# Performance work log

Hardware: AMD Instinct MI355X
Metric: run time of the kernel (lower is better)

The kernel has to match this reference:

```python
import jax, jax.numpy as jnp
import numpy as np

B, D, N, C = 8192, 128, 64, 256

def setup_inputs() -> dict:
    key = jax.random.key(0)
    ks = jax.random.split(key, 7)
    s1 = 1.0 / np.sqrt(D)
    s2 = 1.0 / np.sqrt(C)
    return {
        "X": jax.random.normal(ks[0], (B, D, N), dtype=jnp.float32),
        "W1": jax.random.normal(ks[1], (D, C), dtype=jnp.float32) * s1,
        "b1": jax.random.normal(ks[2], (C,), dtype=jnp.float32) * s1,
        "W2": jax.random.normal(ks[3], (C, C), dtype=jnp.float32) * s2,
        "b2": jax.random.normal(ks[4], (C,), dtype=jnp.float32) * s2,
        "W3": jax.random.normal(ks[5], (C, 1), dtype=jnp.float32) * s2,
        "b3": jax.random.normal(ks[6], (1,), dtype=jnp.float32) * s2,
    }

def reference(X, W1, b1, W2, b2, W3, b3):
    # X: (B, D, N); each per-node slice X[:, :, i] goes through the shared MLP.
    # Batched over nodes: one GEMM instead of N tiny launches.
    h = jax.nn.relu(jnp.einsum('bdn,dc->bnc', X, W1) + b1)   # (B, N, C)
    h = jax.nn.relu(jnp.einsum('bnc,ce->bne', h, W2) + b2)   # (B, N, C)
    logits = jnp.einsum('bnc,co->bno', h, W3) + b3           # (B, N, 1)
    logits = logits[..., 0]                                   # (B, N)
    zeros = jnp.zeros((X.shape[0], 1), dtype=logits.dtype)    # add_zero=True
    return jnp.concatenate([zeros, logits], axis=1)           # (B, N+1)
```

## Files before the change

### kernel.cpp

```cpp
#include <hip/hip_runtime.h>
#include <hip/hip_bf16.h>

typedef unsigned short u16;
typedef unsigned int   u32;
typedef __attribute__((ext_vector_type(8))) short bf16x8;
typedef __attribute__((ext_vector_type(4))) float f32x4;

#define NB 8192

__device__ __forceinline__ u32 pack2bf(float a, float b) {
    __hip_bfloat162 h = __float22bfloat162_rn(make_float2(a, b));
    return *reinterpret_cast<u32*>(&h);
}

__device__ __forceinline__ u16 f2bf(float x) {
    u32 u = __float_as_uint(x);
    u32 r = u + 0x7FFFu + ((u >> 16) & 1u);
    return (u16)(r >> 16);
}

__global__ __launch_bounds__(256) void prep_weights(
    const float* __restrict__ W1, const float* __restrict__ W2,
    u16* __restrict__ w1fr, u16* __restrict__ w2fr)
{
    int tid = blockIdx.x * 256 + threadIdx.x;
    if (tid < 32768) {
        const int f = tid >> 9, r = tid & 511, l = r >> 3, j = r & 7;
        const int wv = f >> 4, mt = (f >> 2) & 3, ks = f & 3;
        const int c = 64 * wv + 16 * mt + (l & 15);
        const int d = 32 * ks + 8 * (l >> 4) + j;
        w1fr[tid] = f2bf(W1[d * 256 + c]);
    } else {
        const int t2 = tid - 32768;
        if (t2 < 65536) {
            const int f = t2 >> 9, r = t2 & 511, l = r >> 3, j = r & 7;
            const int wv = f >> 5, et = (f >> 3) & 3, ks = f & 7;
            const int e = 64 * wv + 16 * et + (l & 15);
            const int c = 32 * ks + 8 * (l >> 4) + j;
            w2fr[t2] = f2bf(W2[c * 256 + e]);
        }
    }
}

__global__ __launch_bounds__(256, 4) void fused_mlp(
    const float* __restrict__ X,
    const float* __restrict__ b1, const float* __restrict__ b2,
    const float* __restrict__ W3, const float* __restrict__ b3,
    const u16* __restrict__ w1fr, const u16* __restrict__ w2fr,
    float* __restrict__ out)
{
    __shared__ u16 smem[64 * 256];
    u16* xt   = smem;
    u16* h1s  = smem;
    float* partl = (float*)smem;

    const int tid = threadIdx.x;
    const int w   = tid >> 6;
    const int l   = tid & 63;
    const int lc  = l & 15;
    const int lk  = l >> 4;
    const int b   = blockIdx.x;
    const float* Xb = X + (size_t)b * 8192;

    const u16* w1b = w1fr + w * 8192  + l * 8;
    const u16* w2b = w2fr + w * 16384 + l * 8;

    #pragma unroll
    for (int it = 0; it < 4; ++it) {
        const int dc = w + 4 * it, d0 = dc << 3;
        float v[8];
        #pragma unroll
        for (int j = 0; j < 8; ++j) v[j] = Xb[(d0 + j) * 64 + l];
        u32 pk[4];
        #pragma unroll
        for (int j = 0; j < 4; ++j) pk[j] = pack2bf(v[2 * j], v[2 * j + 1]);
        *(uint4*)(xt + l * 128 + ((dc ^ lc) << 3)) = make_uint4(pk[0], pk[1], pk[2], pk[3]);
    }

    bf16x8 afrN[4];
    #pragma unroll
    for (int mt = 0; mt < 4; ++mt)
        afrN[mt] = *(const bf16x8*)(w1b + mt * 2048);
    __syncthreads();

    f32x4 acc[4][4];
    #pragma unroll
    for (int mt = 0; mt < 4; ++mt)
        #pragma unroll
        for (int nt = 0; nt < 4; ++nt) acc[mt][nt] = (f32x4){0.f, 0.f, 0.f, 0.f};

    #pragma unroll
    for (int ks = 0; ks < 4; ++ks) {
        bf16x8 afr[4], bfr[4];
        #pragma unroll
        for (int mt = 0; mt < 4; ++mt) afr[mt] = afrN[mt];
        if (ks < 3) {
            #pragma unroll
            for (int mt = 0; mt < 4; ++mt)
                afrN[mt] = *(const bf16x8*)(w1b + (mt * 4 + ks + 1) * 512);
        }
        #pragma unroll
        for (int nt = 0; nt < 4; ++nt)
            bfr[nt] = *(const bf16x8*)(xt + (16 * nt + lc) * 128 + (((4 * ks + lk) ^ lc) << 3));
        #pragma unroll
        for (int mt = 0; mt < 4; ++mt)
            #pragma unroll
            for (int nt = 0; nt < 4; ++nt)
                acc[mt][nt] = __builtin_amdgcn_mfma_f32_16x16x32_bf16(afr[mt], bfr[nt], acc[mt][nt], 0, 0, 0);
    }
    __syncthreads();

    #pragma unroll
    for (int mt = 0; mt < 4; ++mt) {
        const int c0 = 64 * w + 16 * mt + 4 * lk;
        const float4 bv = *(const float4*)(b1 + c0);
        #pragma unroll
        for (int nt = 0; nt < 4; ++nt) {
            const int n = 16 * nt + lc;
            float x0 = fmaxf(acc[mt][nt][0] + bv.x, 0.f);
            float x1 = fmaxf(acc[mt][nt][1] + bv.y, 0.f);
            float x2 = fmaxf(acc[mt][nt][2] + bv.z, 0.f);
            float x3 = fmaxf(acc[mt][nt][3] + bv.w, 0.f);
            const int chunk = (c0 >> 3) ^ lc;
            *(uint2*)(h1s + n * 256 + (chunk << 3) + (c0 & 7)) =
                make_uint2(pack2bf(x0, x1), pack2bf(x2, x3));
        }
    }

    bf16x8 bfrN[4];
    #pragma unroll
    for (int nt = 0; nt < 4; ++nt)
        bfrN[nt] = *(const bf16x8*)(w2b + nt * 4096);
    __syncthreads();

    f32x4 acc2[4][4];
    #pragma unroll
    for (int mt = 0; mt < 4; ++mt)
        #pragma unroll
        for (int nt = 0; nt < 4; ++nt) acc2[mt][nt] = (f32x4){0.f, 0.f, 0.f, 0.f};

    #pragma unroll
    for (int ks = 0; ks < 8; ++ks) {
        bf16x8 afr[4], bfr[4];
        #pragma unroll
        for (int nt = 0; nt < 4; ++nt) bfr[nt] = bfrN[nt];
        if (ks < 7) {
            #pragma unroll
            for (int nt = 0; nt < 4; ++nt)
                bfrN[nt] = *(const bf16x8*)(w2b + (nt * 8 + ks + 1) * 512);
        }
        #pragma unroll
        for (int mt = 0; mt < 4; ++mt)
            afr[mt] = *(const bf16x8*)(h1s + (16 * mt + lc) * 256 + (((4 * ks + lk) ^ lc) << 3));
        #pragma unroll
        for (int mt = 0; mt < 4; ++mt)
            #pragma unroll
            for (int nt = 0; nt < 4; ++nt)
                acc2[mt][nt] = __builtin_amdgcn_mfma_f32_16x16x32_bf16(afr[mt], bfr[nt], acc2[mt][nt], 0, 0, 0);
    }
    __syncthreads();

    float b2v[4], w3v[4];
    #pragma unroll
    for (int nt = 0; nt < 4; ++nt) {
        const int e = 64 * w + 16 * nt + lc;
        b2v[nt] = b2[e];
        w3v[nt] = W3[e];
    }
    #pragma unroll
    for (int mt = 0; mt < 4; ++mt) {
        #pragma unroll
        for (int j = 0; j < 4; ++j) {
            float s = 0.f;
            #pragma unroll
            for (int nt = 0; nt < 4; ++nt)
                s += fmaxf(acc2[mt][nt][j] + b2v[nt], 0.f) * w3v[nt];
            s += __shfl_xor(s, 1);
            s += __shfl_xor(s, 2);
            s += __shfl_xor(s, 4);
            s += __shfl_xor(s, 8);
            if (lc == 0) partl[w * 64 + 16 * mt + 4 * lk + j] = s;
        }
    }
    __syncthreads();

    if (tid < 64) {
        float s = partl[0 * 64 + tid] + partl[1 * 64 + tid] + partl[2 * 64 + tid] + partl[3 * 64 + tid] + b3[0];
        out[(size_t)b * 65 + 1 + tid] = s;
    } else if (tid == 64) {
        out[(size_t)b * 65] = 0.f;
    }
}

extern "C" void kernel_launch(void* const* d_in, const int* in_sizes, int n_in,
                              void* d_out, int out_size, void* d_ws, size_t ws_size,
                              hipStream_t stream) {
    const float* X  = (const float*)d_in[0];
    const float* W1 = (const float*)d_in[1];
    const float* b1 = (const float*)d_in[2];
    const float* W2 = (const float*)d_in[3];
    const float* b2 = (const float*)d_in[4];
    const float* W3 = (const float*)d_in[5];
    const float* b3 = (const float*)d_in[6];
    float* out = (float*)d_out;

    u16* w1fr = (u16*)d_ws;
    u16* w2fr = w1fr + 32768;

    prep_weights<<<384, 256, 0, stream>>>(W1, W2, w1fr, w2fr);
    fused_mlp<<<NB, 256, 0, stream>>>(X, b1, b2, W3, b3, w1fr, w2fr, out);
}
```

Before: 122.2 us.

## Make fused MLP persistent with async global-to-LDS prefetch of next batch

Turns the one-block-per-batch kernel into a persistent kernel with 512 blocks, each looping over 16 batch elements. The next X tile is prefetched straight into LDS with global_load_lds while layer 2 runs, and the bf16 conversion moves into the layer-1 fragment reads. Biases are folded into the accumulator initial values, and MFMA sections get raised wave priority. The aim is to hide X load latency and per-block startup cost, in exchange for more LDS use (fp32 X tile plus a separate h1 buffer), occupancy lowered to 2 blocks, and more LDS reads with conversion inside the GEMM loop.

```diff
diff --git a/kernel.cpp b/kernel.cpp
--- a/kernel.cpp
+++ b/kernel.cpp
@@ -6,7 +6,9 @@
 typedef __attribute__((ext_vector_type(8))) short bf16x8;
 typedef __attribute__((ext_vector_type(4))) float f32x4;
 
-#define NB 8192
+#define NB     8192
+#define GRID_P 512
+#define ITERS  (NB / GRID_P)
 
 __device__ __forceinline__ u32 pack2bf(float a, float b) {
     __hip_bfloat162 h = __float22bfloat162_rn(make_float2(a, b));
@@ -42,124 +44,33 @@
     }
 }
 
-__global__ __launch_bounds__(256, 4) void fused_mlp(
+__global__ __launch_bounds__(256, 2) void fused_mlp(
     const float* __restrict__ X,
     const float* __restrict__ b1, const float* __restrict__ b2,
     const float* __restrict__ W3, const float* __restrict__ b3,
     const u16* __restrict__ w1fr, const u16* __restrict__ w2fr,
     float* __restrict__ out)
 {
-    __shared__ u16 smem[64 * 256];
-    u16* xt   = smem;
-    u16* h1s  = smem;
-    float* partl = (float*)smem;
+    __shared__ __align__(16) float xs[64 * 128];
+    __shared__ __align__(16) u16   h1s[64 * 256];
+    __shared__ float partl[4][64];
 
     const int tid = threadIdx.x;
     const int w   = tid >> 6;
     const int l   = tid & 63;
     const int lc  = l & 15;
     const int lk  = l >> 4;
-    const int b   = blockIdx.x;
-    const float* Xb = X + (size_t)b * 8192;
 
     const u16* w1b = w1fr + w * 8192  + l * 8;
     const u16* w2b = w2fr + w * 16384 + l * 8;
 
-    #pragma unroll
-    for (int it = 0; it < 4; ++it) {
-        const int dc = w + 4 * it, d0 = dc << 3;
-        float v[8];
-        #pragma unroll
-        for (int j = 0; j < 8; ++j) v[j] = Xb[(d0 + j) * 64 + l];
-        u32 pk[4];
-        #pragma unroll
-        for (int j = 0; j < 4; ++j) pk[j] = pack2bf(v[2 * j], v[2 * j + 1]);
-        *(uint4*)(xt + l * 128 + ((dc ^ lc) << 3)) = make_uint4(pk[0], pk[1], pk[2], pk[3]);
-    }
-
-    bf16x8 afrN[4];
+    const int dl = w * 4 + (l >> 4);
+    const int m0 = (l & 15) * 4;
+
+    float4 b1q[4];
     #pragma unroll
     for (int mt = 0; mt < 4; ++mt)
-        afrN[mt] = *(const bf16x8*)(w1b + mt * 2048);
-    __syncthreads();
-
-    f32x4 acc[4][4];
-    #pragma unroll
-    for (int mt = 0; mt < 4; ++mt)
-        #pragma unroll
-        for (int nt = 0; nt < 4; ++nt) acc[mt][nt] = (f32x4){0.f, 0.f, 0.f, 0.f};
-
-    #pragma unroll
-    for (int ks = 0; ks < 4; ++ks) {
-        bf16x8 afr[4], bfr[4];
-        #pragma unroll
-        for (int mt = 0; mt < 4; ++mt) afr[mt] = afrN[mt];
-        if (ks < 3) {
-            #pragma unroll
-            for (int mt = 0; mt < 4; ++mt)
-                afrN[mt] = *(const bf16x8*)(w1b + (mt * 4 + ks + 1) * 512);
-        }
-        #pragma unroll
-        for (int nt = 0; nt < 4; ++nt)
-            bfr[nt] = *(const bf16x8*)(xt + (16 * nt + lc) * 128 + (((4 * ks + lk) ^ lc) << 3));
-        #pragma unroll
-        for (int mt = 0; mt < 4; ++mt)
-            #pragma unroll
-            for (int nt = 0; nt < 4; ++nt)
-                acc[mt][nt] = __builtin_amdgcn_mfma_f32_16x16x32_bf16(afr[mt], bfr[nt], acc[mt][nt], 0, 0, 0);
-    }
-    __syncthreads();
-
-    #pragma unroll
-    for (int mt = 0; mt < 4; ++mt) {
-        const int c0 = 64 * w + 16 * mt + 4 * lk;
-        const float4 bv = *(const float4*)(b1 + c0);
-        #pragma unroll
-        for (int nt = 0; nt < 4; ++nt) {
-            const int n = 16 * nt + lc;
-            float x0 = fmaxf(acc[mt][nt][0] + bv.x, 0.f);
-            float x1 = fmaxf(acc[mt][nt][1] + bv.y, 0.f);
-            float x2 = fmaxf(acc[mt][nt][2] + bv.z, 0.f);
-            float x3 = fmaxf(acc[mt][nt][3] + bv.w, 0.f);
-            const int chunk = (c0 >> 3) ^ lc;
-            *(uint2*)(h1s + n * 256 + (chunk << 3) + (c0 & 7)) =
-                make_uint2(pack2bf(x0, x1), pack2bf(x2, x3));
-        }
-    }
-
-    bf16x8 bfrN[4];
-    #pragma unroll
-    for (int nt = 0; nt < 4; ++nt)
-        bfrN[nt] = *(const bf16x8*)(w2b + nt * 4096);
-    __syncthreads();
-
-    f32x4 acc2[4][4];
-    #pragma unroll
-    for (int mt = 0; mt < 4; ++mt)
-        #pragma unroll
-        for (int nt = 0; nt < 4; ++nt) acc2[mt][nt] = (f32x4){0.f, 0.f, 0.f, 0.f};
-
-    #pragma unroll
-    for (int ks = 0; ks < 8; ++ks) {
-        bf16x8 afr[4], bfr[4];
-        #pragma unroll
-        for (int nt = 0; nt < 4; ++nt) bfr[nt] = bfrN[nt];
-        if (ks < 7) {
-            #pragma unroll
-            for (int nt = 0; nt < 4; ++nt)
-                bfrN[nt] = *(const bf16x8*)(w2b + (nt * 8 + ks + 1) * 512);
-        }
-        #pragma unroll
-        for (int mt = 0; mt < 4; ++mt)
-            afr[mt] = *(const bf16x8*)(h1s + (16 * mt + lc) * 256 + (((4 * ks + lk) ^ lc) << 3));
-        #pragma unroll
-        for (int mt = 0; mt < 4; ++mt)
-            #pragma unroll
-            for (int nt = 0; nt < 4; ++nt)
-                acc2[mt][nt] = __builtin_amdgcn_mfma_f32_16x16x32_bf16(afr[mt], bfr[nt], acc2[mt][nt], 0, 0, 0);
-    }
-    __syncthreads();
-
+        b1q[mt] = *(const float4*)(b1 + 64 * w + 16 * mt + 4 * lk);
     float b2v[4], w3v[4];
     #pragma unroll
     for (int nt = 0; nt < 4; ++nt) {
@@ -167,28 +78,166 @@
         b2v[nt] = b2[e];
         w3v[nt] = W3[e];
     }
-    #pragma unroll
-    for (int mt = 0; mt < 4; ++mt) {
-        #pragma unroll
-        for (int j = 0; j < 4; ++j) {
-            float s = 0.f;
+    const float b3v = b3[0];
+
+    int b = blockIdx.x;
+    {
+        const float* Xb = X + (size_t)b * 8192;
+        #pragma unroll
+        for (int i = 0; i < 8; ++i) {
+            const int d = i * 16 + dl;
+            const float* src = Xb + d * 64 + (m0 ^ (((d >> 3) & 1) << 4));
+            __builtin_amdgcn_global_load_lds(
+                (const __attribute__((address_space(1))) void*)src,
+                (__attribute__((address_space(3))) void*)(xs + i * 1024 + w * 256 + (l & 63) * 4),
+                16, 0, 0);
+        }
+    }
+    __syncthreads();
+
+    #pragma unroll 1
+    for (int it = 0; it < ITERS; ++it, b += GRID_P) {
+        f32x4 acc[4][4];
+        #pragma unroll
+        for (int mt = 0; mt < 4; ++mt)
             #pragma unroll
             for (int nt = 0; nt < 4; ++nt)
-                s += fmaxf(acc2[mt][nt][j] + b2v[nt], 0.f) * w3v[nt];
-            s += __shfl_xor(s, 1);
-            s += __shfl_xor(s, 2);
-            s += __shfl_xor(s, 4);
-            s += __shfl_xor(s, 8);
-            if (lc == 0) partl[w * 64 + 16 * mt + 4 * lk + j] = s;
-        }
-    }
-    __syncthreads();
-
-    if (tid < 64) {
-        float s = partl[0 * 64 + tid] + partl[1 * 64 + tid] + partl[2 * 64 + tid] + partl[3 * 64 + tid] + b3[0];
-        out[(size_t)b * 65 + 1 + tid] = s;
-    } else if (tid == 64) {
-        out[(size_t)b * 65] = 0.f;
+                acc[mt][nt] = (f32x4){b1q[mt].x, b1q[mt].y, b1q[mt].z, b1q[mt].w};
+
+        bf16x8 afrN[4];
+        #pragma unroll
+        for (int mt = 0; mt < 4; ++mt)
+            afrN[mt] = *(const bf16x8*)(w1b + mt * 2048);
+
+        const int px = (lk & 1) << 4;
+        #pragma unroll
+        for (int ks = 0; ks < 4; ++ks) {
+            bf16x8 afr[4], bfr[4];
+            #pragma unroll
+            for (int mt = 0; mt < 4; ++mt) afr[mt] = afrN[mt];
+            if (ks < 3) {
+                #pragma unroll
+                for (int mt = 0; mt < 4; ++mt)
+                    afrN[mt] = *(const bf16x8*)(w1b + (mt * 4 + ks + 1) * 512);
+            }
+            #pragma unroll
+            for (int nt = 0; nt < 4; ++nt) {
+                const int col = (16 * nt + lc) ^ px;
+                const int rb  = (32 * ks + 8 * lk) * 64 + col;
+                float xv[8];
+                #pragma unroll
+                for (int j = 0; j < 8; ++j) xv[j] = xs[rb + j * 64];
+                union { bf16x8 v; u32 d[4]; } fr;
+                #pragma unroll
+                for (int j = 0; j < 4; ++j) fr.d[j] = pack2bf(xv[2 * j], xv[2 * j + 1]);
+                bfr[nt] = fr.v;
+            }
+            __builtin_amdgcn_s_setprio(1);
+            #pragma unroll
+            for (int mt = 0; mt < 4; ++mt)
+                #pragma unroll
+                for (int nt = 0; nt < 4; ++nt)
+                    acc[mt][nt] = __builtin_amdgcn_mfma_f32_16x16x32_bf16(afr[mt], bfr[nt], acc[mt][nt], 0, 0, 0);
+            __builtin_amdgcn_s_setprio(0);
+        }
+        __syncthreads();
+
+        const int bn = b + GRID_P;
+        if (bn < NB) {
+            const float* Xb = X + (size_t)bn * 8192;
+            #pragma unroll
+            for (int i = 0; i < 8; ++i) {
+                const int d = i * 16 + dl;
+                const float* src = Xb + d * 64 + (m0 ^ (((d >> 3) & 1) << 4));
+                __builtin_amdgcn_global_load_lds(
+                    (const __attribute__((address_space(1))) void*)src,
+                    (__attribute__((address_space(3))) void*)(xs + i * 1024 + w * 256 + (l & 63) * 4),
+                    16, 0, 0);
+            }
+        }
+
+        #pragma unroll
+        for (int mt = 0; mt < 4; ++mt) {
+            const int c0 = 64 * w + 16 * mt + 4 * lk;
+            #pragma unroll
+            for (int nt = 0; nt < 4; ++nt) {
+                const int n = 16 * nt + lc;
+                float x0 = fmaxf(acc[mt][nt][0], 0.f);
+                float x1 = fmaxf(acc[mt][nt][1], 0.f);
+                float x2 = fmaxf(acc[mt][nt][2], 0.f);
+                float x3 = fmaxf(acc[mt][nt][3], 0.f);
+                const int chunk = (c0 >> 3) ^ lc;
+                *(uint2*)(h1s + n * 256 + (chunk << 3) + (c0 & 7)) =
+                    make_uint2(pack2bf(x0, x1), pack2bf(x2, x3));
+            }
+        }
+
+        asm volatile("s_waitcnt lgkmcnt(0)" ::: "memory");
+        __builtin_amdgcn_s_barrier();
+        asm volatile("" ::: "memory");
+
+        f32x4 acc2[4][4];
+        #pragma unroll
+        for (int mt = 0; mt < 4; ++mt)
+            #pragma unroll
+            for (int nt = 0; nt < 4; ++nt)
+                acc2[mt][nt] = (f32x4){b2v[nt], b2v[nt], b2v[nt], b2v[nt]};
+
+        bf16x8 bfrN[4];
+        #pragma unroll
+        for (int nt = 0; nt < 4; ++nt)
+            bfrN[nt] = *(const bf16x8*)(w2b + nt * 4096);
+
+        #pragma unroll
+        for (int ks = 0; ks < 8; ++ks) {
+            bf16x8 afr[4], bfr[4];
+            #pragma unroll
+            for (int nt = 0; nt < 4; ++nt) bfr[nt] = bfrN[nt];
+            if (ks < 7) {
+                #pragma unroll
+                for (int nt = 0; nt < 4; ++nt)
+                    bfrN[nt] = *(const bf16x8*)(w2b + (nt * 8 + ks + 1) * 512);
+            }
+            #pragma unroll
+            for (int mt = 0; mt < 4; ++mt)
+                afr[mt] = *(const bf16x8*)(h1s + (16 * mt + lc) * 256 + (((4 * ks + lk) ^ lc) << 3));
+            __builtin_amdgcn_s_setprio(1);
+            #pragma unroll
+            for (int mt = 0; mt < 4; ++mt)
+                #pragma unroll
+                for (int nt = 0; nt < 4; ++nt)
+                    acc2[mt][nt] = __builtin_amdgcn_mfma_f32_16x16x32_bf16(afr[mt], bfr[nt], acc2[mt][nt], 0, 0, 0);
+            __builtin_amdgcn_s_setprio(0);
+        }
+
+        #pragma unroll
+        for (int mt = 0; mt < 4; ++mt) {
+            #pragma unroll
+            for (int j = 0; j < 4; ++j) {
+                float s = 0.f;
+                #pragma unroll
+                for (int nt = 0; nt < 4; ++nt)
+                    s += fmaxf(acc2[mt][nt][j], 0.f) * w3v[nt];
+                s += __shfl_xor(s, 1);
+                s += __shfl_xor(s, 2);
+                s += __shfl_xor(s, 4);
+                s += __shfl_xor(s, 8);
+                if (lc == 0) partl[w][16 * mt + 4 * lk + j] = s;
+            }
+        }
+
+        asm volatile("s_waitcnt lgkmcnt(0)" ::: "memory");
+        __builtin_amdgcn_s_barrier();
+        asm volatile("" ::: "memory");
+
+        if (tid < 64) {
+            float s = partl[0][tid] + partl[1][tid] + partl[2][tid] + partl[3][tid] + b3v;
+            out[(size_t)b * 65 + 1 + tid] = s;
+        } else if (tid == 64) {
+            out[(size_t)b * 65] = 0.f;
+        }
+
+        __syncthreads();
     }
 }
 
@@ -208,5 +257,5 @@
     u16* w2fr = w1fr + 32768;
 
     prep_weights<<<384, 256, 0, stream>>>(W1, W2, w1fr, w2fr);
-    fused_mlp<<<NB, 256, 0, stream>>>(X, b1, b2, W3, b3, w1fr, w2fr, out);
-}
+    fused_mlp<<<GRID_P, 256, 0, stream>>>(X, b1, b2, W3, b3, w1fr, w2fr, out);
+}
```

Result: slower. 302.5 us (+147.6%).

## Convert fused MLP into persistent producer/consumer warp-specialized pipeline

Applied to the files above, without the earlier changes.

Replaces the one-block-per-batch kernel with 256 persistent 1024-thread blocks that loop over batches. Even waves compute layer 1 and prefetch the next X tile into a double-buffered LDS slot. Odd waves compute layer 2 plus the W3 reduction on the previous h1 buffer, and one wave writes the output two steps behind. Biases are folded into the accumulator initialisation and MFMA sections are marked with setprio. The aim is to overlap X loading with matrix math, but it uses 100KB of LDS per block, only 256 blocks on the device, and a block-wide barrier every step.

```diff
diff --git a/kernel.cpp b/kernel.cpp
--- a/kernel.cpp
+++ b/kernel.cpp
@@ -6,7 +6,9 @@
 typedef __attribute__((ext_vector_type(8))) short bf16x8;
 typedef __attribute__((ext_vector_type(4))) float f32x4;
 
-#define NB 8192
+#define NB    8192
+#define NBLK  256
+#define STEPS (NB / NBLK)
 
 __device__ __forceinline__ u32 pack2bf(float a, float b) {
     __hip_bfloat162 h = __float22bfloat162_rn(make_float2(a, b));
@@ -26,169 +28,213 @@
     int tid = blockIdx.x * 256 + threadIdx.x;
     if (tid < 32768) {
         const int f = tid >> 9, r = tid & 511, l = r >> 3, j = r & 7;
-        const int wv = f >> 4, mt = (f >> 2) & 3, ks = f & 3;
-        const int c = 64 * wv + 16 * mt + (l & 15);
+        const int p = f >> 3, mt = (f >> 2) & 1, ks = f & 3;
+        const int c = 32 * p + 16 * mt + (l & 15);
         const int d = 32 * ks + 8 * (l >> 4) + j;
         w1fr[tid] = f2bf(W1[d * 256 + c]);
     } else {
         const int t2 = tid - 32768;
         if (t2 < 65536) {
             const int f = t2 >> 9, r = t2 & 511, l = r >> 3, j = r & 7;
-            const int wv = f >> 5, et = (f >> 3) & 3, ks = f & 7;
-            const int e = 64 * wv + 16 * et + (l & 15);
-            const int c = 32 * ks + 8 * (l >> 4) + j;
-            w2fr[t2] = f2bf(W2[c * 256 + e]);
-        }
-    }
-}
-
-__global__ __launch_bounds__(256, 4) void fused_mlp(
+            const int q = f >> 4, et = (f >> 3) & 1, ks = f & 7;
+            const int e = 32 * q + 16 * et + (l & 15);
+            const int cc = 32 * ks + 8 * (l >> 4) + j;
+            w2fr[t2] = f2bf(W2[cc * 256 + e]);
+        }
+    }
+}
+
+__global__ __launch_bounds__(1024, 4) void pc_mlp(
     const float* __restrict__ X,
     const float* __restrict__ b1, const float* __restrict__ b2,
     const float* __restrict__ W3, const float* __restrict__ b3,
     const u16* __restrict__ w1fr, const u16* __restrict__ w2fr,
     float* __restrict__ out)
 {
-    __shared__ u16 smem[64 * 256];
-    u16* xt   = smem;
-    u16* h1s  = smem;
-    float* partl = (float*)smem;
+    extern __shared__ __align__(16) u16 smem[];
+    u16*   const xt0   = smem;
+    u16*   const h10   = smem + 16384;
+    float* const partl = (float*)(smem + 49152);
 
     const int tid = threadIdx.x;
-    const int w   = tid >> 6;
+    const int wv  = tid >> 6;
     const int l   = tid & 63;
     const int lc  = l & 15;
     const int lk  = l >> 4;
-    const int b   = blockIdx.x;
-    const float* Xb = X + (size_t)b * 8192;
-
-    const u16* w1b = w1fr + w * 8192  + l * 8;
-    const u16* w2b = w2fr + w * 16384 + l * 8;
-
-    #pragma unroll
-    for (int it = 0; it < 4; ++it) {
-        const int dc = w + 4 * it, d0 = dc << 3;
-        float v[8];
+    const bool isProd = (wv & 1) == 0;
+    const int rid = wv >> 1;
+    const int bk  = blockIdx.x;
+
+    float4 b1q[2];
+    const u16* w1b = w1fr + rid * 4096 + l * 8;
+    float b2v[2], w3v[2];
+    const u16* w2b = w2fr + rid * 8192 + l * 8;
+    float b3v = 0.f;
+    if (isProd) {
         #pragma unroll
-        for (int j = 0; j < 8; ++j) v[j] = Xb[(d0 + j) * 64 + l];
-        u32 pk[4];
+        for (int mt = 0; mt < 2; ++mt)
+            b1q[mt] = *(const float4*)(b1 + 32 * rid + 16 * mt + 4 * lk);
+    } else {
         #pragma unroll
-        for (int j = 0; j < 4; ++j) pk[j] = pack2bf(v[2 * j], v[2 * j + 1]);
-        *(uint4*)(xt + l * 128 + ((dc ^ lc) << 3)) = make_uint4(pk[0], pk[1], pk[2], pk[3]);
-    }
-
-    bf16x8 afrN[4];
-    #pragma unroll
-    for (int mt = 0; mt < 4; ++mt)
-        afrN[mt] = *(const bf16x8*)(w1b + mt * 2048);
+        for (int et = 0; et < 2; ++et) {
+            const int e = 32 * rid + 16 * et + lc;
+            b2v[et] = b2[e];
+            w3v[et] = W3[e];
+        }
+        b3v = b3[0];
+    }
+
+    if (isProd) {
+        const float* Xb = X + (size_t)bk * 8192;
+        #pragma unroll
+        for (int c2 = 0; c2 < 2; ++c2) {
+            const int dc = rid + 8 * c2, d0 = dc << 3;
+            float v[8];
+            #pragma unroll
+            for (int j = 0; j < 8; ++j) v[j] = Xb[(d0 + j) * 64 + l];
+            u32 pk[4];
+            #pragma unroll
+            for (int j = 0; j < 4; ++j) pk[j] = pack2bf(v[2 * j], v[2 * j + 1]);
+            *(uint4*)(xt0 + l * 128 + ((dc ^ lc) << 3)) = make_uint4(pk[0], pk[1], pk[2], pk[3]);
+        }
+    }
     __syncthreads();
 
-    f32x4 acc[4][4];
-    #pragma unroll
-    for (int mt = 0; mt < 4; ++mt)
-        #pragma unroll
-        for (int nt = 0; nt < 4; ++nt) acc[mt][nt] = (f32x4){0.f, 0.f, 0.f, 0.f};
-
-    #pragma unroll
-    for (int ks = 0; ks < 4; ++ks) {
-        bf16x8 afr[4], bfr[4];
-        #pragma unroll
-        for (int mt = 0; mt < 4; ++mt) afr[mt] = afrN[mt];
-        if (ks < 3) {
-            #pragma unroll
-            for (int mt = 0; mt < 4; ++mt)
-                afrN[mt] = *(const bf16x8*)(w1b + (mt * 4 + ks + 1) * 512);
-        }
-        #pragma unroll
-        for (int nt = 0; nt < 4; ++nt)
-            bfr[nt] = *(const bf16x8*)(xt + (16 * nt + lc) * 128 + (((4 * ks + lk) ^ lc) << 3));
-        #pragma unroll
-        for (int mt = 0; mt < 4; ++mt)
-            #pragma unroll
-            for (int nt = 0; nt < 4; ++nt)
-                acc[mt][nt] = __builtin_amdgcn_mfma_f32_16x16x32_bf16(afr[mt], bfr[nt], acc[mt][nt], 0, 0, 0);
-    }
-    __syncthreads();
-
-    #pragma unroll
-    for (int mt = 0; mt < 4; ++mt) {
-        const int c0 = 64 * w + 16 * mt + 4 * lk;
-        const float4 bv = *(const float4*)(b1 + c0);
-        #pragma unroll
-        for (int nt = 0; nt < 4; ++nt) {
-            const int n = 16 * nt + lc;
-            float x0 = fmaxf(acc[mt][nt][0] + bv.x, 0.f);
-            float x1 = fmaxf(acc[mt][nt][1] + bv.y, 0.f);
-            float x2 = fmaxf(acc[mt][nt][2] + bv.z, 0.f);
-            float x3 = fmaxf(acc[mt][nt][3] + bv.w, 0.f);
-            const int chunk = (c0 >> 3) ^ lc;
-            *(uint2*)(h1s + n * 256 + (chunk << 3) + (c0 & 7)) =
-                make_uint2(pack2bf(x0, x1), pack2bf(x2, x3));
-        }
-    }
-
-    bf16x8 bfrN[4];
-    #pragma unroll
-    for (int nt = 0; nt < 4; ++nt)
-        bfrN[nt] = *(const bf16x8*)(w2b + nt * 4096);
-    __syncthreads();
-
-    f32x4 acc2[4][4];
-    #pragma unroll
-    for (int mt = 0; mt < 4; ++mt)
-        #pragma unroll
-        for (int nt = 0; nt < 4; ++nt) acc2[mt][nt] = (f32x4){0.f, 0.f, 0.f, 0.f};
-
-    #pragma unroll
-    for (int ks = 0; ks < 8; ++ks) {
-        bf16x8 afr[4], bfr[4];
-        #pragma unroll
-        for (int nt = 0; nt < 4; ++nt) bfr[nt] = bfrN[nt];
-        if (ks < 7) {
-            #pragma unroll
-            for (int nt = 0; nt < 4; ++nt)
-                bfrN[nt] = *(const bf16x8*)(w2b + (nt * 8 + ks + 1) * 512);
-        }
-        #pragma unroll
-        for (int mt = 0; mt < 4; ++mt)
-            afr[mt] = *(const bf16x8*)(h1s + (16 * mt + lc) * 256 + (((4 * ks + lk) ^ lc) << 3));
-        #pragma unroll
-        for (int mt = 0; mt < 4; ++mt)
-            #pragma unroll
-            for (int nt = 0; nt < 4; ++nt)
-                acc2[mt][nt] = __builtin_amdgcn_mfma_f32_16x16x32_bf16(afr[mt], bfr[nt], acc2[mt][nt], 0, 0, 0);
-    }
-    __syncthreads();
-
-    float b2v[4], w3v[4];
-    #pragma unroll
-    for (int nt = 0; nt < 4; ++nt) {
-        const int e = 64 * w + 16 * nt + lc;
-        b2v[nt] = b2[e];
-        w3v[nt] = W3[e];
-    }
-    #pragma unroll
-    for (int mt = 0; mt < 4; ++mt) {
-        #pragma unroll
-        for (int j = 0; j < 4; ++j) {
-            float s = 0.f;
-            #pragma unroll
-            for (int nt = 0; nt < 4; ++nt)
-                s += fmaxf(acc2[mt][nt][j] + b2v[nt], 0.f) * w3v[nt];
-            s += __shfl_xor(s, 1);
-            s += __shfl_xor(s, 2);
-            s += __shfl_xor(s, 4);
-            s += __shfl_xor(s, 8);
-            if (lc == 0) partl[w * 64 + 16 * mt + 4 * lk + j] = s;
-        }
-    }
-    __syncthreads();
-
-    if (tid < 64) {
-        float s = partl[0 * 64 + tid] + partl[1 * 64 + tid] + partl[2 * 64 + tid] + partl[3 * 64 + tid] + b3[0];
-        out[(size_t)b * 65 + 1 + tid] = s;
-    } else if (tid == 64) {
-        out[(size_t)b * 65] = 0.f;
+    #pragma unroll 1
+    for (int it = 0; it < STEPS + 2; ++it) {
+        if (isProd) {
+            if (it < STEPS) {
+                const int b = bk + it * NBLK;
+                float v[2][8];
+                if (it < STEPS - 1) {
+                    const float* Xn = X + (size_t)(b + NBLK) * 8192;
+                    #pragma unroll
+                    for (int c2 = 0; c2 < 2; ++c2) {
+                        const int d0 = (rid + 8 * c2) << 3;
+                        #pragma unroll
+                        for (int j = 0; j < 8; ++j) v[c2][j] = Xn[(d0 + j) * 64 + l];
+                    }
+                }
+                const u16* xb = xt0 + (it & 1) * 8192;
+                f32x4 acc[2][4];
+                #pragma unroll
+                for (int mt = 0; mt < 2; ++mt)
+                    #pragma unroll
+                    for (int nt = 0; nt < 4; ++nt)
+                        acc[mt][nt] = (f32x4){b1q[mt].x, b1q[mt].y, b1q[mt].z, b1q[mt].w};
+                bf16x8 afrN[2];
+                #pragma unroll
+                for (int mt = 0; mt < 2; ++mt)
+                    afrN[mt] = *(const bf16x8*)(w1b + mt * 2048);
+                #pragma unroll
+                for (int ks = 0; ks < 4; ++ks) {
+                    bf16x8 afr[2], bfr[4];
+                    #pragma unroll
+                    for (int mt = 0; mt < 2; ++mt) afr[mt] = afrN[mt];
+                    if (ks < 3) {
+                        #pragma unroll
+                        for (int mt = 0; mt < 2; ++mt)
+                            afrN[mt] = *(const bf16x8*)(w1b + (mt * 4 + ks + 1) * 512);
+                    }
+                    #pragma unroll
+                    for (int nt = 0; nt < 4; ++nt)
+                        bfr[nt] = *(const bf16x8*)(xb + (16 * nt + lc) * 128 + (((4 * ks + lk) ^ lc) << 3));
+                    __builtin_amdgcn_s_setprio(1);
+                    #pragma unroll
+                    for (int mt = 0; mt < 2; ++mt)
+                        #pragma unroll
+                        for (int nt = 0; nt < 4; ++nt)
+                            acc[mt][nt] = __builtin_amdgcn_mfma_f32_16x16x32_bf16(afr[mt], bfr[nt], acc[mt][nt], 0, 0, 0);
+                    __builtin_amdgcn_s_setprio(0);
+                }
+                u16* hw = h10 + (it & 1) * 16384;
+                #pragma unroll
+                for (int mt = 0; mt < 2; ++mt) {
+                    const int c0 = 32 * rid + 16 * mt + 4 * lk;
+                    #pragma unroll
+                    for (int nt = 0; nt < 4; ++nt) {
+                        const int n = 16 * nt + lc;
+                        float x0 = fmaxf(acc[mt][nt][0], 0.f);
+                        float x1 = fmaxf(acc[mt][nt][1], 0.f);
+                        float x2 = fmaxf(acc[mt][nt][2], 0.f);
+                        float x3 = fmaxf(acc[mt][nt][3], 0.f);
+                        const int chunk = (c0 >> 3) ^ lc;
+                        *(uint2*)(hw + n * 256 + (chunk << 3) + (c0 & 7)) =
+                            make_uint2(pack2bf(x0, x1), pack2bf(x2, x3));
+                    }
+                }
+                if (it < STEPS - 1) {
+                    u16* xn = xt0 + ((it + 1) & 1) * 8192;
+                    #pragma unroll
+                    for (int c2 = 0; c2 < 2; ++c2) {
+                        const int dc = rid + 8 * c2;
+                        u32 pk[4];
+                        #pragma unroll
+                        for (int j = 0; j < 4; ++j) pk[j] = pack2bf(v[c2][2 * j], v[c2][2 * j + 1]);
+                        *(uint4*)(xn + l * 128 + ((dc ^ lc) << 3)) = make_uint4(pk[0], pk[1], pk[2], pk[3]);
+                    }
+                }
+            }
+        } else {
+            if (it >= 2 && it <= STEPS + 1 && wv == 1) {
+                const int bo = bk + (it - 2) * NBLK;
+                const float* pr = partl + ((it - 1) & 1) * 512;
+                float s = b3v;
+                #pragma unroll
+                for (int k = 0; k < 8; ++k) s += pr[k * 64 + l];
+                out[(size_t)bo * 65 + 1 + l] = s;
+                if (l == 0) out[(size_t)bo * 65] = 0.f;
+            }
+            if (it >= 1 && it <= STEPS) {
+                const u16* hb = h10 + ((it - 1) & 1) * 16384;
+                f32x4 acc2[4][2];
+                #pragma unroll
+                for (int mt = 0; mt < 4; ++mt)
+                    #pragma unroll
+                    for (int et = 0; et < 2; ++et)
+                        acc2[mt][et] = (f32x4){b2v[et], b2v[et], b2v[et], b2v[et]};
+                bf16x8 bfrN[2];
+                #pragma unroll
+                for (int et = 0; et < 2; ++et)
+                    bfrN[et] = *(const bf16x8*)(w2b + et * 4096);
+                #pragma unroll
+                for (int ks = 0; ks < 8; ++ks) {
+                    bf16x8 afr[4], bfr[2];
+                    #pragma unroll
+                    for (int et = 0; et < 2; ++et) bfr[et] = bfrN[et];
+                    if (ks < 7) {
+                        #pragma unroll
+                        for (int et = 0; et < 2; ++et)
+                            bfrN[et] = *(const bf16x8*)(w2b + (et * 8 + ks + 1) * 512);
+                    }
+                    #pragma unroll
+                    for (int mt = 0; mt < 4; ++mt)
+                        afr[mt] = *(const bf16x8*)(hb + (16 * mt + lc) * 256 + (((4 * ks + lk) ^ lc) << 3));
+                    __builtin_amdgcn_s_setprio(1);
+                    #pragma unroll
+                    for (int mt = 0; mt < 4; ++mt)
+                        #pragma unroll
+                        for (int et = 0; et < 2; ++et)
+                            acc2[mt][et] = __builtin_amdgcn_mfma_f32_16x16x32_bf16(afr[mt], bfr[et], acc2[mt][et], 0, 0, 0);
+                    __builtin_amdgcn_s_setprio(0);
+                }
+                float* pw = partl + (it & 1) * 512 + rid * 64;
+                #pragma unroll
+                for (int mt = 0; mt < 4; ++mt) {
+                    #pragma unroll
+                    for (int j = 0; j < 4; ++j) {
+                        float s = fmaxf(acc2[mt][0][j], 0.f) * w3v[0]
+                                + fmaxf(acc2[mt][1][j], 0.f) * w3v[1];
+                        s += __shfl_xor(s, 1);
+                        s += __shfl_xor(s, 2);
+                        s += __shfl_xor(s, 4);
+                        s += __shfl_xor(s, 8);
+                        if (lc == 0) pw[16 * mt + 4 * lk + j] = s;
+                    }
+                }
+            }
+        }
+        __syncthreads();
     }
 }
 
@@ -208,5 +254,5 @@
     u16* w2fr = w1fr + 32768;
 
     prep_weights<<<384, 256, 0, stream>>>(W1, W2, w1fr, w2fr);
-    fused_mlp<<<NB, 256, 0, stream>>>(X, b1, b2, W3, b3, w1fr, w2fr, out);
-}
+    pc_mlp<<<NBLK, 1024, 102400, stream>>>(X, b1, b2, W3, b3, w1fr, w2fr, out);
+}
```

Result: slower. 447.8 us (+266.6%).

## Load X fragments directly into registers, skipping LDS staging; fold biases into accumulators

Applied to the files above, without the earlier changes.

The first GEMM now builds its X operand fragments straight from global memory in registers. Each 32-d slice is converted to bf16 and fed to MFMA as it arrives, so the LDS transpose buffer and two barriers are gone. Biases b1 and b2 are preloaded into the accumulators instead of being added in the epilogue, and partl gets its own shared array. In exchange, every wave re-reads the whole X tile from global/L2, four times the global traffic per block, with strided 4-byte loads. The grid size is also derived from the input size.

```diff
diff --git a/kernel.cpp b/kernel.cpp
--- a/kernel.cpp
+++ b/kernel.cpp
@@ -49,10 +49,8 @@
     const u16* __restrict__ w1fr, const u16* __restrict__ w2fr,
     float* __restrict__ out)
 {
-    __shared__ u16 smem[64 * 256];
-    u16* xt   = smem;
-    u16* h1s  = smem;
-    float* partl = (float*)smem;
+    __shared__ __align__(16) u16 h1s[64 * 256];
+    __shared__ float partl[4][64];
 
     const int tid = threadIdx.x;
     const int w   = tid >> 6;
@@ -65,79 +63,82 @@
     const u16* w1b = w1fr + w * 8192  + l * 8;
     const u16* w2b = w2fr + w * 16384 + l * 8;
 
-    #pragma unroll
-    for (int it = 0; it < 4; ++it) {
-        const int dc = w + 4 * it, d0 = dc << 3;
-        float v[8];
-        #pragma unroll
-        for (int j = 0; j < 8; ++j) v[j] = Xb[(d0 + j) * 64 + l];
-        u32 pk[4];
-        #pragma unroll
-        for (int j = 0; j < 4; ++j) pk[j] = pack2bf(v[2 * j], v[2 * j + 1]);
-        *(uint4*)(xt + l * 128 + ((dc ^ lc) << 3)) = make_uint4(pk[0], pk[1], pk[2], pk[3]);
-    }
-
-    bf16x8 afrN[4];
-    #pragma unroll
-    for (int mt = 0; mt < 4; ++mt)
-        afrN[mt] = *(const bf16x8*)(w1b + mt * 2048);
-    __syncthreads();
-
     f32x4 acc[4][4];
     #pragma unroll
-    for (int mt = 0; mt < 4; ++mt)
-        #pragma unroll
-        for (int nt = 0; nt < 4; ++nt) acc[mt][nt] = (f32x4){0.f, 0.f, 0.f, 0.f};
+    for (int mt = 0; mt < 4; ++mt) {
+        const float4 bq = *(const float4*)(b1 + 64 * w + 16 * mt + 4 * lk);
+        #pragma unroll
+        for (int nt = 0; nt < 4; ++nt)
+            acc[mt][nt] = (f32x4){bq.x, bq.y, bq.z, bq.w};
+    }
+
+    const float* xbase = Xb + (8 * lk) * 64 + lc;
 
     #pragma unroll
     for (int ks = 0; ks < 4; ++ks) {
-        bf16x8 afr[4], bfr[4];
-        #pragma unroll
-        for (int mt = 0; mt < 4; ++mt) afr[mt] = afrN[mt];
-        if (ks < 3) {
+        bf16x8 afr[4];
+        #pragma unroll
+        for (int mt = 0; mt < 4; ++mt)
+            afr[mt] = *(const bf16x8*)(w1b + (mt * 4 + ks) * 512);
+
+        const float* xp = xbase + ks * 2048;
+        #pragma unroll
+        for (int pr = 0; pr < 2; ++pr) {
+            float xv[2][8];
+            #pragma unroll
+            for (int t = 0; t < 2; ++t) {
+                const int nt = 2 * pr + t;
+                #pragma unroll
+                for (int j = 0; j < 8; ++j)
+                    xv[t][j] = xp[j * 64 + nt * 16];
+            }
+            bf16x8 bfr[2];
+            #pragma unroll
+            for (int t = 0; t < 2; ++t) {
+                union { bf16x8 v; u32 d[4]; } fr;
+                #pragma unroll
+                for (int j = 0; j < 4; ++j) fr.d[j] = pack2bf(xv[t][2 * j], xv[t][2 * j + 1]);
+                bfr[t] = fr.v;
+            }
             #pragma unroll
             for (int mt = 0; mt < 4; ++mt)
-                afrN[mt] = *(const bf16x8*)(w1b + (mt * 4 + ks + 1) * 512);
-        }
-        #pragma unroll
-        for (int nt = 0; nt < 4; ++nt)
-            bfr[nt] = *(const bf16x8*)(xt + (16 * nt + lc) * 128 + (((4 * ks + lk) ^ lc) << 3));
-        #pragma unroll
-        for (int mt = 0; mt < 4; ++mt)
-            #pragma unroll
-            for (int nt = 0; nt < 4; ++nt)
-                acc[mt][nt] = __builtin_amdgcn_mfma_f32_16x16x32_bf16(afr[mt], bfr[nt], acc[mt][nt], 0, 0, 0);
-    }
-    __syncthreads();
+                #pragma unroll
+                for (int t = 0; t < 2; ++t)
+                    acc[mt][2 * pr + t] = __builtin_amdgcn_mfma_f32_16x16x32_bf16(
+                        afr[mt], bfr[t], acc[mt][2 * pr + t], 0, 0, 0);
+        }
+    }
 
     #pragma unroll
     for (int mt = 0; mt < 4; ++mt) {
         const int c0 = 64 * w + 16 * mt + 4 * lk;
-        const float4 bv = *(const float4*)(b1 + c0);
         #pragma unroll
         for (int nt = 0; nt < 4; ++nt) {
             const int n = 16 * nt + lc;
-            float x0 = fmaxf(acc[mt][nt][0] + bv.x, 0.f);
-            float x1 = fmaxf(acc[mt][nt][1] + bv.y, 0.f);
-            float x2 = fmaxf(acc[mt][nt][2] + bv.z, 0.f);
-            float x3 = fmaxf(acc[mt][nt][3] + bv.w, 0.f);
+            float x0 = fmaxf(acc[mt][nt][0], 0.f);
+            float x1 = fmaxf(acc[mt][nt][1], 0.f);
+            float x2 = fmaxf(acc[mt][nt][2], 0.f);
+            float x3 = fmaxf(acc[mt][nt][3], 0.f);
             const int chunk = (c0 >> 3) ^ lc;
             *(uint2*)(h1s + n * 256 + (chunk << 3) + (c0 & 7)) =
                 make_uint2(pack2bf(x0, x1), pack2bf(x2, x3));
         }
     }
+    __syncthreads();
+
+    f32x4 acc2[4][4];
+    #pragma unroll
+    for (int nt = 0; nt < 4; ++nt) {
+        const float bv = b2[64 * w + 16 * nt + lc];
+        #pragma unroll
+        for (int mt = 0; mt < 4; ++mt)
+            acc2[mt][nt] = (f32x4){bv, bv, bv, bv};
+    }
 
     bf16x8 bfrN[4];
     #pragma unroll
     for (int nt = 0; nt < 4; ++nt)
         bfrN[nt] = *(const bf16x8*)(w2b + nt * 4096);
-    __syncthreads();
-
-    f32x4 acc2[4][4];
-    #pragma unroll
-    for (int mt = 0; mt < 4; ++mt)
-        #pragma unroll
-        for (int nt = 0; nt < 4; ++nt) acc2[mt][nt] = (f32x4){0.f, 0.f, 0.f, 0.f};
 
     #pragma unroll
     for (int ks = 0; ks < 8; ++ks) {
@@ -158,15 +159,12 @@
             for (int nt = 0; nt < 4; ++nt)
                 acc2[mt][nt] = __builtin_amdgcn_mfma_f32_16x16x32_bf16(afr[mt], bfr[nt], acc2[mt][nt], 0, 0, 0);
     }
-    __syncthreads();
-
-    float b2v[4], w3v[4];
-    #pragma unroll
-    for (int nt = 0; nt < 4; ++nt) {
-        const int e = 64 * w + 16 * nt + lc;
-        b2v[nt] = b2[e];
-        w3v[nt] = W3[e];
-    }
+
+    float w3v[4];
+    #pragma unroll
+    for (int nt = 0; nt < 4; ++nt)
+        w3v[nt] = W3[64 * w + 16 * nt + lc];
+
     #pragma unroll
     for (int mt = 0; mt < 4; ++mt) {
         #pragma unroll
@@ -174,18 +172,18 @@
             float s = 0.f;
             #pragma unroll
             for (int nt = 0; nt < 4; ++nt)
-                s += fmaxf(acc2[mt][nt][j] + b2v[nt], 0.f) * w3v[nt];
+                s += fmaxf(acc2[mt][nt][j], 0.f) * w3v[nt];
             s += __shfl_xor(s, 1);
             s += __shfl_xor(s, 2);
             s += __shfl_xor(s, 4);
             s += __shfl_xor(s, 8);
-            if (lc == 0) partl[w * 64 + 16 * mt + 4 * lk + j] = s;
+            if (lc == 0) partl[w][16 * mt + 4 * lk + j] = s;
         }
     }
     __syncthreads();
 
     if (tid < 64) {
-        float s = partl[0 * 64 + tid] + partl[1 * 64 + tid] + partl[2 * 64 + tid] + partl[3 * 64 + tid] + b3[0];
+        float s = partl[0][tid] + partl[1][tid] + partl[2][tid] + partl[3][tid] + b3[0];
         out[(size_t)b * 65 + 1 + tid] = s;
     } else if (tid == 64) {
         out[(size_t)b * 65] = 0.f;
@@ -207,6 +205,8 @@
     u16* w1fr = (u16*)d_ws;
     u16* w2fr = w1fr + 32768;
 
+    const int B = in_sizes[0] / (128 * 64);
+
     prep_weights<<<384, 256, 0, stream>>>(W1, W2, w1fr, w2fr);
-    fused_mlp<<<NB, 256, 0, stream>>>(X, b1, b2, W3, b3, w1fr, w2fr, out);
-}
+    fused_mlp<<<B, 256, 0, stream>>>(X, b1, b2, W3, b3, w1fr, w2fr, out);
+}
```

Measured after the change: 170.3 us. +39.4%, slower.
